# Optimization experiments

Measured on AMD Instinct MI355X. Metric: run time of the kernel, lower is better.

## Reference

```python
import jax, jax.numpy as jnp
import numpy as np

NUM_NODES = 1_000_000
HID = 256
OUT = 128


def _sage_layer(h, src, dst, n_dst, W_self, W_neigh, b):
    # DGL SAGEConv('mean'): mean-aggregate neighbor msgs, then fc_neigh + fc_self + bias
    msgs = h[src]                                                  # [E, F] gather
    sums = jax.ops.segment_sum(msgs, dst, num_segments=n_dst)      # [n_dst, F]
    deg = jax.ops.segment_sum(jnp.ones((src.shape[0],), h.dtype), dst, num_segments=n_dst)
    mean = sums / jnp.maximum(deg, 1.0)[:, None]                   # zero-degree -> 0
    h_self = h[:n_dst]                                             # DGL block: dst = first n_dst src
    return h_self @ W_self + mean @ W_neigh + b


def setup_inputs() -> dict:
    key = jax.random.key(0)
    ks = jax.random.split(key, 12)
    N0, N1, N2 = 1_048_576, 65_536, 4_096
    E0, E1 = 1_048_576, 65_536
    inp = {
        "input_nodes": jax.random.randint(ks[0], (N0,), 0, NUM_NODES),
        "src0": jax.random.randint(ks[1], (E0,), 0, N0),
        "dst0": jax.random.randint(ks[2], (E0,), 0, N1),
        "src1": jax.random.randint(ks[3], (E1,), 0, N1),
        "dst1": jax.random.randint(ks[4], (E1,), 0, N2),
        "n_dst0": N1,
        "n_dst1": N2,
        "embed_table": jax.random.normal(ks[5], (NUM_NODES, HID), jnp.float32),
        "W_self0": jax.random.normal(ks[6], (HID, HID), jnp.float32) / np.sqrt(HID),
        "W_neigh0": jax.random.normal(ks[7], (HID, HID), jnp.float32) / np.sqrt(HID),
        "b0": jnp.zeros((HID,), jnp.float32),
        "W_self1": jax.random.normal(ks[8], (HID, OUT), jnp.float32) / np.sqrt(HID),
        "W_neigh1": jax.random.normal(ks[9], (HID, OUT), jnp.float32) / np.sqrt(HID),
        "b1": jnp.zeros((OUT,), jnp.float32),
    }
    return inp


def reference(input_nodes, src0, dst0, src1, dst1, n_dst0, n_dst1,
              embed_table, W_self0, W_neigh0, b0, W_self1, W_neigh1, b1):
    h = embed_table[input_nodes]                       # [N0, HID] embedding lookup
    h = _sage_layer(h, src0, dst0, n_dst0, W_self0, W_neigh0, b0)
    h = jax.nn.relu(h)                                 # dropout is identity in eval mode
    h = _sage_layer(h, src1, dst1, n_dst1, W_self1, W_neigh1, b1)
    return h                                           # [4096, OUT]
```

## Files before the change

kernel.cpp:

```cpp
#include <hip/hip_runtime.h>
#include <hip/hip_bf16.h>
#include <cstddef>
#include <cstdint>


#define HID 256

using f32x4  = __attribute__((ext_vector_type(4))) float;
using bf16x8 = __attribute__((ext_vector_type(8))) short;
using u16x8  = __attribute__((ext_vector_type(8))) unsigned short;

static __device__ __forceinline__ ushort f2bf(float f) {
    union { float f; unsigned u; } v; v.f = f;
    unsigned r = v.u + 0x7FFF + ((v.u >> 16) & 1);
    return (ushort)(r >> 16);
}
static __device__ __forceinline__ float bf2f(ushort h) {
    union { unsigned u; float f; } v; v.u = ((unsigned)h) << 16;
    return v.f;
}

__global__ __launch_bounds__(256) void edge_hist(
    const int* __restrict__ dst, int* __restrict__ cnt, int E)
{
    int i = blockIdx.x * 256 + threadIdx.x;
    if (i < E) atomicAdd(&cnt[dst[i]], 1);
}

__global__ __launch_bounds__(256) void scan_block(
    const int* __restrict__ cnt, int* __restrict__ offs, int* __restrict__ totals)
{
    __shared__ int sh[256];
    int t = threadIdx.x;
    int i = blockIdx.x * 256 + t;
    int v = cnt[i];
    sh[t] = v;
    __syncthreads();
    #pragma unroll
    for (int d = 1; d < 256; d <<= 1) {
        int x = (t >= d) ? sh[t - d] : 0;
        __syncthreads();
        sh[t] += x;
        __syncthreads();
    }
    offs[i] = sh[t] - v;
    if (t == 255) totals[blockIdx.x] = sh[t];
}

__global__ __launch_bounds__(256) void scan_totals(
    int* __restrict__ totals, int nb)
{
    __shared__ int sh[256];
    int t = threadIdx.x;
    int v = (t < nb) ? totals[t] : 0;
    sh[t] = v;
    __syncthreads();
    #pragma unroll
    for (int d = 1; d < 256; d <<= 1) {
        int x = (t >= d) ? sh[t - d] : 0;
        __syncthreads();
        sh[t] += x;
        __syncthreads();
    }
    if (t < nb) totals[t] = sh[t] - v;
}

__global__ __launch_bounds__(256) void scan_add(
    int* __restrict__ offs, const int* __restrict__ totals,
    int* __restrict__ cursor, int n, int E)
{
    int i = blockIdx.x * 256 + threadIdx.x;
    if (i < n) {
        int v = offs[i] + totals[i >> 8];
        offs[i] = v;
        cursor[i] = v;
    }
    if (i == 0) offs[n] = E;
}

template<bool RESOLVE>
__global__ __launch_bounds__(256) void edge_scatter(
    const int* __restrict__ src, const int* __restrict__ dst,
    const int* __restrict__ node_idx,
    int* __restrict__ cursor, int* __restrict__ edge_rows, int E)
{
    int i = blockIdx.x * 256 + threadIdx.x;
    if (i < E) {
        int d = dst[i];
        int pos = atomicAdd(&cursor[d], 1);
        int s = src[i];
        edge_rows[pos] = RESOLVE ? node_idx[s] : s;
    }
}

template<bool SRC_F32>
__global__ __launch_bounds__(256) void sage_gather_mean(
    const void* __restrict__ table,
    const int* __restrict__ offs,
    const int* __restrict__ edge_rows,
    ushort* __restrict__ mean_out,
    int n_dst)
{
    int w = blockIdx.x * 4 + (threadIdx.x >> 6);
    int lane = threadIdx.x & 63;
    if (w >= n_dst) return;
    int beg = offs[w], end = offs[w + 1];
    float a0 = 0.f, a1 = 0.f, a2 = 0.f, a3 = 0.f;
    int e = beg;
    while (e < end) {
        int cnt = end - e; cnt = cnt > 8 ? 8 : cnt;
        int myrow = 0;
        if (lane < cnt) myrow = edge_rows[e + lane];
        f32x4  vf[8];
        ushort4 vh[8];
        #pragma unroll
        for (int j = 0; j < 8; ++j) {
            if (j < cnt) {
                int r = __shfl(myrow, j);
                if (SRC_F32)
                    vf[j] = *((const f32x4*)((const float*)table + (size_t)r * HID) + lane);
                else
                    vh[j] = *((const ushort4*)((const ushort*)table + (size_t)r * HID) + lane);
            }
        }
        #pragma unroll
        for (int j = 0; j < 8; ++j) {
            if (j < cnt) {
                if (SRC_F32) { a0 += vf[j].x; a1 += vf[j].y; a2 += vf[j].z; a3 += vf[j].w; }
                else { a0 += bf2f(vh[j].x); a1 += bf2f(vh[j].y); a2 += bf2f(vh[j].z); a3 += bf2f(vh[j].w); }
            }
        }
        e += cnt;
    }
    float inv = 1.0f / (float)max(end - beg, 1);
    ushort4 o;
    o.x = f2bf(a0 * inv); o.y = f2bf(a1 * inv);
    o.z = f2bf(a2 * inv); o.w = f2bf(a3 * inv);
    *((ushort4*)(mean_out + (size_t)w * HID) + lane) = o;
}

__global__ __launch_bounds__(256) void build_wt(
    const float* __restrict__ Wself, const float* __restrict__ Wneigh,
    ushort* __restrict__ WT, int N)
{
    int i = blockIdx.x * 256 + threadIdx.x;
    if (i >= N * 512) return;
    int n = i >> 9;
    int k = i & 511;
    float v = (k < HID) ? Wself[(size_t)k * N + n]
                        : Wneigh[(size_t)(k - HID) * N + n];
    WT[i] = f2bf(v);
}

template<int BN, bool RELU, bool GATHER, bool SELF_F32, bool OUT_BF16>
__global__ __launch_bounds__(256) void sage_gemm_mfma(
    const void* __restrict__ Aself,
    const int* __restrict__ idx,
    const ushort* __restrict__ Amean,
    const ushort* __restrict__ WT,
    const float* __restrict__ bias,
    void* __restrict__ Out)
{
    constexpr int BM = 64, BK = 64;
    constexpr int WN = BN / 64;
    constexpr int WM = 4 / WN;
    constexpr int M_FR = (BM / WM) / 16;

    __shared__ __align__(16) ushort As[BM * BK];
    __shared__ __align__(16) ushort Bs[BN * BK];

    const int t = threadIdx.x;
    const int brow = blockIdx.x * BM;
    const int w = t >> 6, l = t & 63;
    const int wc = (w % WN) * 64;
    const int wr = (w / WN) * (BM / WM);
    const int l15 = l & 15, l4 = l >> 4;

    f32x4 acc[M_FR][4] = {};

    for (int k0 = 0; k0 < 2 * HID; k0 += BK) {
        const bool self = (k0 < HID);

        if (self && SELF_F32) {
            #pragma unroll
            for (int i = 0; i < 4; ++i) {
                int li = t + i * 256;
                int r  = li >> 4;
                int k4 = (li & 15) << 2;
                size_t rg = GATHER ? (size_t)idx[brow + r] : (size_t)(brow + r);
                f32x4 v = *(const f32x4*)((const float*)Aself + rg * HID + k0 + k4);
                ushort4 h;
                h.x = f2bf(v.x); h.y = f2bf(v.y); h.z = f2bf(v.z); h.w = f2bf(v.w);
                *(ushort4*)&As[(r * BK + k4) ^ ((r & 7) << 3)] = h;
            }
        } else {
            #pragma unroll
            for (int i = 0; i < 2; ++i) {
                int li = t + i * 256;
                int r  = li >> 3;
                int k8 = (li & 7) << 3;
                const ushort* sp;
                if (self) {
                    size_t rg = GATHER ? (size_t)idx[brow + r] : (size_t)(brow + r);
                    sp = (const ushort*)Aself + rg * HID + k0 + k8;
                } else {
                    sp = Amean + (size_t)(brow + r) * HID + (k0 - HID) + k8;
                }
                *(u16x8*)&As[(r * BK + k8) ^ ((r & 7) << 3)] = *(const u16x8*)sp;
            }
        }

        #pragma unroll
        for (int i = 0; i < BN / 32; ++i) {
            int li = t + i * 256;
            int n  = li >> 3;
            int k8 = (li & 7) << 3;
            *(u16x8*)&Bs[(n * BK + k8) ^ ((n & 7) << 3)] =
                *(const u16x8*)(WT + (size_t)n * 512 + k0 + k8);
        }
        __syncthreads();

        #pragma unroll
        for (int kk = 0; kk < 2; ++kk) {
            int koff = kk * 32 + l4 * 8;
            bf16x8 a[M_FR], b[4];
            #pragma unroll
            for (int m = 0; m < M_FR; ++m) {
                int r = wr + m * 16 + l15;
                a[m] = *(const bf16x8*)&As[(r * BK + koff) ^ ((r & 7) << 3)];
            }
            #pragma unroll
            for (int n = 0; n < 4; ++n) {
                int c = wc + n * 16 + l15;
                b[n] = *(const bf16x8*)&Bs[(c * BK + koff) ^ ((c & 7) << 3)];
            }
            #pragma unroll
            for (int m = 0; m < M_FR; ++m)
                #pragma unroll
                for (int n = 0; n < 4; ++n)
                    acc[m][n] = __builtin_amdgcn_mfma_f32_16x16x32_bf16(
                        a[m], b[n], acc[m][n], 0, 0, 0);
        }
        __syncthreads();
    }

    #pragma unroll
    for (int m = 0; m < M_FR; ++m) {
        #pragma unroll
        for (int n = 0; n < 4; ++n) {
            int col = wc + n * 16 + l15;
            float bv = bias[col];
            #pragma unroll
            for (int r = 0; r < 4; ++r) {
                int row = brow + wr + m * 16 + l4 * 4 + r;
                float v = acc[m][n][r] + bv;
                if (RELU) v = fmaxf(v, 0.f);
                if (OUT_BF16) ((ushort*)Out)[(size_t)row * BN + col] = f2bf(v);
                else          ((float*)Out)[(size_t)row * BN + col] = v;
            }
        }
    }
}

extern "C" void kernel_launch(void* const* d_in, const int* in_sizes, int n_in,
                              void* d_out, int out_size, void* d_ws, size_t ws_size,
                              hipStream_t stream) {
    const int*   input_nodes = (const int*)d_in[0];
    const int*   src0        = (const int*)d_in[1];
    const int*   dst0        = (const int*)d_in[2];
    const int*   src1        = (const int*)d_in[3];
    const int*   dst1        = (const int*)d_in[4];
    const float* embed       = (const float*)d_in[7];
    const float* W_self0     = (const float*)d_in[8];
    const float* W_neigh0    = (const float*)d_in[9];
    const float* b0          = (const float*)d_in[10];
    const float* W_self1     = (const float*)d_in[11];
    const float* W_neigh1    = (const float*)d_in[12];
    const float* b1          = (const float*)d_in[13];
    float*       out         = (float*)d_out;

    const int E0 = in_sizes[1];
    const int E1 = in_sizes[3];
    const int N1 = 65536;
    const int N2 = 4096;

    char* ws = (char*)d_ws;
    ushort* mean0  = (ushort*)(ws + ((size_t)0  << 20));
    ushort* h1     = (ushort*)(ws + ((size_t)32 << 20));
    int*    edges0 = (int*)  (ws + ((size_t)64 << 20));
    int*    edges1 = (int*)  (ws + ((size_t)68 << 20));
    int*    cnt0   = (int*)  (ws + ((size_t)69 << 20));
    int*    offs0  = (int*)  (ws + ((size_t)70 << 20));
    int*    cnt1   = (int*)  (ws + ((size_t)71 << 20));
    int*    offs1  = (int*)  (ws + ((size_t)72 << 20));
    int*    tot0   = (int*)  (ws + ((size_t)73 << 20));
    int*    tot1   = (int*)  (ws + ((size_t)73 << 20) + 4096);
    ushort* WT0    = (ushort*)(ws + ((size_t)74 << 20));
    ushort* WT1    = (ushort*)(ws + ((size_t)75 << 20));
    ushort* mean1  = (ushort*)(ws + ((size_t)76 << 20));

    build_wt<<<512, 256, 0, stream>>>(W_self0, W_neigh0, WT0, 256);
    build_wt<<<256, 256, 0, stream>>>(W_self1, W_neigh1, WT1, 128);

    hipMemsetAsync(cnt0, 0, (size_t)N1 * 4, stream);
    edge_hist<<<(E0 + 255) / 256, 256, 0, stream>>>(dst0, cnt0, E0);
    scan_block<<<N1 / 256, 256, 0, stream>>>(cnt0, offs0, tot0);
    scan_totals<<<1, 256, 0, stream>>>(tot0, N1 / 256);
    scan_add<<<N1 / 256, 256, 0, stream>>>(offs0, tot0, cnt0, N1, E0);
    edge_scatter<true><<<(E0 + 255) / 256, 256, 0, stream>>>(
        src0, dst0, input_nodes, cnt0, edges0, E0);
    sage_gather_mean<true><<<N1 / 4, 256, 0, stream>>>(
        embed, offs0, edges0, mean0, N1);
    sage_gemm_mfma<256, true, true, true, true><<<N1 / 64, 256, 0, stream>>>(
        embed, input_nodes, mean0, WT0, b0, h1);

    hipMemsetAsync(cnt1, 0, (size_t)N2 * 4, stream);
    edge_hist<<<(E1 + 255) / 256, 256, 0, stream>>>(dst1, cnt1, E1);
    scan_block<<<N2 / 256, 256, 0, stream>>>(cnt1, offs1, tot1);
    scan_totals<<<1, 256, 0, stream>>>(tot1, N2 / 256);
    scan_add<<<N2 / 256, 256, 0, stream>>>(offs1, tot1, cnt1, N2, E1);
    edge_scatter<false><<<(E1 + 255) / 256, 256, 0, stream>>>(
        src1, dst1, nullptr, cnt1, edges1, E1);
    sage_gather_mean<false><<<N2 / 4, 256, 0, stream>>>(
        h1, offs1, edges1, mean1, N2);
    sage_gemm_mfma<128, false, false, false, false><<<N2 / 64, 256, 0, stream>>>(
        h1, nullptr, mean1, WT1, b1, out);
}
```

Baseline: 409.7 us.

## Merge both layers' CSR build into one pass and register-prefetch GEMM tiles

Both layers' edge histogram, scan and scatter now run as single combined launches over a concatenated node range, and the two weight-transpose kernels become one launch. This cuts the number of small kernel launches and memsets. Separately, the MFMA GEMM now loads the next K-step's A and B tiles into registers while the current step computes, then stores them to LDS after a barrier. That adds register pressure and an extra barrier per step.

```diff
diff --git a/kernel.cpp b/kernel.cpp
--- a/kernel.cpp
+++ b/kernel.cpp
@@ -5,6 +5,8 @@
 
 
 #define HID 256
+#define N1 65536
+#define N2 4096
 
 using f32x4  = __attribute__((ext_vector_type(4))) float;
 using bf16x8 = __attribute__((ext_vector_type(8))) short;
@@ -20,11 +22,31 @@
     return v.f;
 }
 
-__global__ __launch_bounds__(256) void edge_hist(
-    const int* __restrict__ dst, int* __restrict__ cnt, int E)
+__global__ __launch_bounds__(256) void build_wt01(
+    const float* __restrict__ Ws0, const float* __restrict__ Wn0,
+    const float* __restrict__ Ws1, const float* __restrict__ Wn1,
+    ushort* __restrict__ WT0, ushort* __restrict__ WT1)
 {
     int i = blockIdx.x * 256 + threadIdx.x;
-    if (i < E) atomicAdd(&cnt[dst[i]], 1);
+    if (i < 256 * 512) {
+        int n = i >> 9, k = i & 511;
+        float v = (k < HID) ? Ws0[(size_t)k * 256 + n] : Wn0[(size_t)(k - HID) * 256 + n];
+        WT0[i] = f2bf(v);
+    } else {
+        int j = i - 256 * 512;
+        int n = j >> 9, k = j & 511;
+        float v = (k < HID) ? Ws1[(size_t)k * 128 + n] : Wn1[(size_t)(k - HID) * 128 + n];
+        WT1[j] = f2bf(v);
+    }
+}
+
+__global__ __launch_bounds__(256) void edge_hist01(
+    const int* __restrict__ dst0, const int* __restrict__ dst1,
+    int* __restrict__ cnt01, int E0, int E1)
+{
+    int i = blockIdx.x * 256 + threadIdx.x;
+    if (i < E0) atomicAdd(&cnt01[dst0[i]], 1);
+    else if (i < E0 + E1) atomicAdd(&cnt01[N1 + dst1[i - E0]], 1);
 }
 
 __global__ __launch_bounds__(256) void scan_block(
@@ -47,16 +69,16 @@
     if (t == 255) totals[blockIdx.x] = sh[t];
 }
 
-__global__ __launch_bounds__(256) void scan_totals(
+__global__ __launch_bounds__(512) void scan_totals(
     int* __restrict__ totals, int nb)
 {
-    __shared__ int sh[256];
+    __shared__ int sh[512];
     int t = threadIdx.x;
     int v = (t < nb) ? totals[t] : 0;
     sh[t] = v;
     __syncthreads();
     #pragma unroll
-    for (int d = 1; d < 256; d <<= 1) {
+    for (int d = 1; d < 512; d <<= 1) {
         int x = (t >= d) ? sh[t - d] : 0;
         __syncthreads();
         sh[t] += x;
@@ -67,7 +89,7 @@
 
 __global__ __launch_bounds__(256) void scan_add(
     int* __restrict__ offs, const int* __restrict__ totals,
-    int* __restrict__ cursor, int n, int E)
+    int* __restrict__ cursor, int n, int total_edges)
 {
     int i = blockIdx.x * 256 + threadIdx.x;
     if (i < n) {
@@ -75,21 +97,23 @@
         offs[i] = v;
         cursor[i] = v;
     }
-    if (i == 0) offs[n] = E;
-}
-
-template<bool RESOLVE>
-__global__ __launch_bounds__(256) void edge_scatter(
-    const int* __restrict__ src, const int* __restrict__ dst,
+    if (i == 0) offs[n] = total_edges;
+}
+
+__global__ __launch_bounds__(256) void edge_scatter01(
+    const int* __restrict__ src0, const int* __restrict__ dst0,
+    const int* __restrict__ src1, const int* __restrict__ dst1,
     const int* __restrict__ node_idx,
-    int* __restrict__ cursor, int* __restrict__ edge_rows, int E)
+    int* __restrict__ cursor, int* __restrict__ edge_rows, int E0, int E1)
 {
     int i = blockIdx.x * 256 + threadIdx.x;
-    if (i < E) {
-        int d = dst[i];
-        int pos = atomicAdd(&cursor[d], 1);
-        int s = src[i];
-        edge_rows[pos] = RESOLVE ? node_idx[s] : s;
+    if (i < E0) {
+        int pos = atomicAdd(&cursor[dst0[i]], 1);
+        edge_rows[pos] = node_idx[src0[i]];
+    } else if (i < E0 + E1) {
+        int e = i - E0;
+        int pos = atomicAdd(&cursor[N1 + dst1[e]], 1);
+        edge_rows[pos] = src1[e];
     }
 }
 
@@ -139,19 +163,6 @@
     *((ushort4*)(mean_out + (size_t)w * HID) + lane) = o;
 }
 
-__global__ __launch_bounds__(256) void build_wt(
-    const float* __restrict__ Wself, const float* __restrict__ Wneigh,
-    ushort* __restrict__ WT, int N)
-{
-    int i = blockIdx.x * 256 + threadIdx.x;
-    if (i >= N * 512) return;
-    int n = i >> 9;
-    int k = i & 511;
-    float v = (k < HID) ? Wself[(size_t)k * N + n]
-                        : Wneigh[(size_t)(k - HID) * N + n];
-    WT[i] = f2bf(v);
-}
-
 template<int BN, bool RELU, bool GATHER, bool SELF_F32, bool OUT_BF16>
 __global__ __launch_bounds__(256) void sage_gemm_mfma(
     const void* __restrict__ Aself,
@@ -177,48 +188,70 @@
     const int l15 = l & 15, l4 = l >> 4;
 
     f32x4 acc[M_FR][4] = {};
-
-    for (int k0 = 0; k0 < 2 * HID; k0 += BK) {
-        const bool self = (k0 < HID);
-
-        if (self && SELF_F32) {
+    f32x4 af[4];
+    u16x8 ah[2];
+    u16x8 bh[BN / 32];
+
+    auto load_step = [&](int k0) {
+        if (SELF_F32 && k0 < HID) {
             #pragma unroll
             for (int i = 0; i < 4; ++i) {
-                int li = t + i * 256;
-                int r  = li >> 4;
-                int k4 = (li & 15) << 2;
+                int li = t + i * 256; int r = li >> 4; int k4 = (li & 15) << 2;
                 size_t rg = GATHER ? (size_t)idx[brow + r] : (size_t)(brow + r);
-                f32x4 v = *(const f32x4*)((const float*)Aself + rg * HID + k0 + k4);
-                ushort4 h;
-                h.x = f2bf(v.x); h.y = f2bf(v.y); h.z = f2bf(v.z); h.w = f2bf(v.w);
-                *(ushort4*)&As[(r * BK + k4) ^ ((r & 7) << 3)] = h;
+                af[i] = *(const f32x4*)((const float*)Aself + rg * HID + k0 + k4);
             }
         } else {
             #pragma unroll
             for (int i = 0; i < 2; ++i) {
-                int li = t + i * 256;
-                int r  = li >> 3;
-                int k8 = (li & 7) << 3;
+                int li = t + i * 256; int r = li >> 3; int k8 = (li & 7) << 3;
                 const ushort* sp;
-                if (self) {
+                if (k0 < HID) {
                     size_t rg = GATHER ? (size_t)idx[brow + r] : (size_t)(brow + r);
                     sp = (const ushort*)Aself + rg * HID + k0 + k8;
                 } else {
                     sp = Amean + (size_t)(brow + r) * HID + (k0 - HID) + k8;
                 }
-                *(u16x8*)&As[(r * BK + k8) ^ ((r & 7) << 3)] = *(const u16x8*)sp;
-            }
-        }
-
+                ah[i] = *(const u16x8*)sp;
+            }
+        }
         #pragma unroll
         for (int i = 0; i < BN / 32; ++i) {
-            int li = t + i * 256;
-            int n  = li >> 3;
-            int k8 = (li & 7) << 3;
-            *(u16x8*)&Bs[(n * BK + k8) ^ ((n & 7) << 3)] =
-                *(const u16x8*)(WT + (size_t)n * 512 + k0 + k8);
-        }
-        __syncthreads();
+            int li = t + i * 256; int n = li >> 3; int k8 = (li & 7) << 3;
+            bh[i] = *(const u16x8*)(WT + (size_t)n * 512 + k0 + k8);
+        }
+    };
+
+    auto store_step = [&](int k0) {
+        if (SELF_F32 && k0 < HID) {
+            #pragma unroll
+            for (int i = 0; i < 4; ++i) {
+                int li = t + i * 256; int r = li >> 4; int k4 = (li & 15) << 2;
+                ushort4 h;
+                h.x = f2bf(af[i].x); h.y = f2bf(af[i].y);
+                h.z = f2bf(af[i].z); h.w = f2bf(af[i].w);
+                *(ushort4*)&As[(r * BK + k4) ^ ((r & 7) << 3)] = h;
+            }
+        } else {
+            #pragma unroll
+            for (int i = 0; i < 2; ++i) {
+                int li = t + i * 256; int r = li >> 3; int k8 = (li & 7) << 3;
+                *(u16x8*)&As[(r * BK + k8) ^ ((r & 7) << 3)] = ah[i];
+            }
+        }
+        #pragma unroll
+        for (int i = 0; i < BN / 32; ++i) {
+            int li = t + i * 256; int n = li >> 3; int k8 = (li & 7) << 3;
+            *(u16x8*)&Bs[(n * BK + k8) ^ ((n & 7) << 3)] = bh[i];
+        }
+    };
+
+    load_step(0);
+    store_step(0);
+    __syncthreads();
+
+    for (int k0 = 0; k0 < 2 * HID; k0 += BK) {
+        int kn = k0 + BK;
+        if (kn < 2 * HID) load_step(kn);
 
         #pragma unroll
         for (int kk = 0; kk < 2; ++kk) {
@@ -241,6 +274,8 @@
                     acc[m][n] = __builtin_amdgcn_mfma_f32_16x16x32_bf16(
                         a[m], b[n], acc[m][n], 0, 0, 0);
         }
+        __syncthreads();
+        if (kn < 2 * HID) store_step(kn);
         __syncthreads();
     }
 
@@ -281,48 +316,35 @@
 
     const int E0 = in_sizes[1];
     const int E1 = in_sizes[3];
-    const int N1 = 65536;
-    const int N2 = 4096;
+    const int NC = N1 + N2;
 
     char* ws = (char*)d_ws;
-    ushort* mean0  = (ushort*)(ws + ((size_t)0  << 20));
-    ushort* h1     = (ushort*)(ws + ((size_t)32 << 20));
-    int*    edges0 = (int*)  (ws + ((size_t)64 << 20));
-    int*    edges1 = (int*)  (ws + ((size_t)68 << 20));
-    int*    cnt0   = (int*)  (ws + ((size_t)69 << 20));
-    int*    offs0  = (int*)  (ws + ((size_t)70 << 20));
-    int*    cnt1   = (int*)  (ws + ((size_t)71 << 20));
-    int*    offs1  = (int*)  (ws + ((size_t)72 << 20));
-    int*    tot0   = (int*)  (ws + ((size_t)73 << 20));
-    int*    tot1   = (int*)  (ws + ((size_t)73 << 20) + 4096);
-    ushort* WT0    = (ushort*)(ws + ((size_t)74 << 20));
-    ushort* WT1    = (ushort*)(ws + ((size_t)75 << 20));
-    ushort* mean1  = (ushort*)(ws + ((size_t)76 << 20));
-
-    build_wt<<<512, 256, 0, stream>>>(W_self0, W_neigh0, WT0, 256);
-    build_wt<<<256, 256, 0, stream>>>(W_self1, W_neigh1, WT1, 128);
-
-    hipMemsetAsync(cnt0, 0, (size_t)N1 * 4, stream);
-    edge_hist<<<(E0 + 255) / 256, 256, 0, stream>>>(dst0, cnt0, E0);
-    scan_block<<<N1 / 256, 256, 0, stream>>>(cnt0, offs0, tot0);
-    scan_totals<<<1, 256, 0, stream>>>(tot0, N1 / 256);
-    scan_add<<<N1 / 256, 256, 0, stream>>>(offs0, tot0, cnt0, N1, E0);
-    edge_scatter<true><<<(E0 + 255) / 256, 256, 0, stream>>>(
-        src0, dst0, input_nodes, cnt0, edges0, E0);
+    ushort* mean0   = (ushort*)(ws + ((size_t)0  << 20));
+    ushort* h1      = (ushort*)(ws + ((size_t)32 << 20));
+    int*    edges01 = (int*)  (ws + ((size_t)64 << 20));
+    int*    cnt01   = (int*)  (ws + ((size_t)70 << 20));
+    int*    tot01   = cnt01 + NC;
+    int*    offs01  = (int*)  (ws + ((size_t)71 << 20));
+    ushort* WT0     = (ushort*)(ws + ((size_t)72 << 20));
+    ushort* WT1     = (ushort*)(ws + ((size_t)73 << 20));
+    ushort* mean1   = (ushort*)(ws + ((size_t)74 << 20));
+
+    hipMemsetAsync(cnt01, 0, (size_t)(NC + 272) * 4, stream);
+    build_wt01<<<768, 256, 0, stream>>>(W_self0, W_neigh0, W_self1, W_neigh1, WT0, WT1);
+    edge_hist01<<<(E0 + E1 + 255) / 256, 256, 0, stream>>>(dst0, dst1, cnt01, E0, E1);
+    scan_block<<<NC / 256, 256, 0, stream>>>(cnt01, offs01, tot01);
+    scan_totals<<<1, 512, 0, stream>>>(tot01, NC / 256);
+    scan_add<<<NC / 256, 256, 0, stream>>>(offs01, tot01, cnt01, NC, E0 + E1);
+    edge_scatter01<<<(E0 + E1 + 255) / 256, 256, 0, stream>>>(
+        src0, dst0, src1, dst1, input_nodes, cnt01, edges01, E0, E1);
+
     sage_gather_mean<true><<<N1 / 4, 256, 0, stream>>>(
-        embed, offs0, edges0, mean0, N1);
+        embed, offs01, edges01, mean0, N1);
     sage_gemm_mfma<256, true, true, true, true><<<N1 / 64, 256, 0, stream>>>(
         embed, input_nodes, mean0, WT0, b0, h1);
 
-    hipMemsetAsync(cnt1, 0, (size_t)N2 * 4, stream);
-    edge_hist<<<(E1 + 255) / 256, 256, 0, stream>>>(dst1, cnt1, E1);
-    scan_block<<<N2 / 256, 256, 0, stream>>>(cnt1, offs1, tot1);
-    scan_totals<<<1, 256, 0, stream>>>(tot1, N2 / 256);
-    scan_add<<<N2 / 256, 256, 0, stream>>>(offs1, tot1, cnt1, N2, E1);
-    edge_scatter<false><<<(E1 + 255) / 256, 256, 0, stream>>>(
-        src1, dst1, nullptr, cnt1, edges1, E1);
     sage_gather_mean<false><<<N2 / 4, 256, 0, stream>>>(
-        h1, offs1, edges1, mean1, N2);
+        h1, offs01 + N1, edges01, mean1, N2);
     sage_gemm_mfma<128, false, false, false, false><<<N2 / 64, 256, 0, stream>>>(
         h1, nullptr, mean1, WT1, b1, out);
 }
```

Result: faster. 340.0 us (-17.0%).
